# Performance work log

Measured on AMD Instinct MI355X. Metric: run time of the kernel, lower is better.

Reference implementation:

```python
import jax, jax.numpy as jnp
import numpy as np

IN_CH = 512
MID = max(IN_CH // 8, 1)


def setup_inputs() -> dict:
    key = jax.random.key(0)
    ks = jax.random.split(key, 8)
    B, C, H, W = 4, IN_CH, 64, 64
    s = 0.05
    x = jax.random.normal(ks[0], (B, C, H, W), dtype=jnp.float32)
    wq = jax.random.normal(ks[1], (MID, C), dtype=jnp.float32) * s
    bq = jnp.zeros((MID,), dtype=jnp.float32)
    wk = jax.random.normal(ks[2], (MID, C), dtype=jnp.float32) * s
    bk = jnp.zeros((MID,), dtype=jnp.float32)
    wv = jax.random.normal(ks[3], (C, C), dtype=jnp.float32) * s
    bv = jnp.zeros((C,), dtype=jnp.float32)
    alpha = jnp.ones((1,), dtype=jnp.float32) * 0.5  # nonzero so attention path is exercised
    return {"x": x, "wq": wq, "bq": bq, "wk": wk, "bk": bk, "wv": wv, "bv": bv, "alpha": alpha}


def reference(x, wq, bq, wk, bk, wv, bv, alpha):
    B, C, H, W = x.shape
    N = H * W
    xf = x.reshape(B, C, N)  # [B, C, N]
    # 1x1 convs == per-position channel GEMMs
    q = jnp.einsum('mc,bcn->bnm', wq, xf) + bq  # [B, N, mid]
    k = jnp.einsum('mc,bcn->bmn', wk, xf) + bk[None, :, None]  # [B, mid, N]
    v = jnp.einsum('dc,bcn->bdn', wv, xf) + bv[None, :, None]  # [B, C, N]
    attn = jax.nn.softmax(jnp.einsum('bnm,bmk->bnk', q, k), axis=-1)  # [B, N, N]
    out = jnp.einsum('bdn,bkn->bdk', v, attn)  # v @ attn^T -> [B, C, N]
    out = out.reshape(B, C, H, W)
    return alpha * out + x
```

## Files before the change

### kernel.cpp

```cpp
#include <hip/hip_runtime.h>

#define BB 4
#define CD 512
#define NP 4096
#define MID 64
#define PSTR 88

typedef _Float16 half8 __attribute__((ext_vector_type(8)));
typedef _Float16 half4 __attribute__((ext_vector_type(4)));
typedef float floatx4 __attribute__((ext_vector_type(4)));

#define LOG2E 1.4426950408889634f

__global__ __launch_bounds__(256) void prep_w(
    const float* __restrict__ wq, const float* __restrict__ wk,
    const float* __restrict__ wv, const float* __restrict__ bq,
    const float* __restrict__ bk, const float* __restrict__ bv,
    _Float16* __restrict__ w_h, float* __restrict__ bias) {
  int idx = blockIdx.x * 256 + threadIdx.x;
  for (int i = idx; i < 640 * 512; i += gridDim.x * 256) {
    int r = i >> 9, c = i & 511;
    float v = (r < 64) ? wq[(r << 9) + c] * LOG2E
            : (r < 128) ? wk[((r - 64) << 9) + c]
                        : wv[((r - 128) << 9) + c];
    w_h[i] = (_Float16)v;
  }
  if (idx < 640) {
    float v = (idx < 64) ? bq[idx] * LOG2E
            : (idx < 128) ? bk[idx - 64]
                          : bv[idx - 128];
    bias[idx] = v;
  }
}

__global__ __launch_bounds__(256) void transpose_x(const float* __restrict__ x,
                                                   _Float16* __restrict__ xt) {
  __shared__ float tile[64][65];
  int b = blockIdx.z, c0 = blockIdx.y * 64, n0 = blockIdx.x * 64;
  int t = threadIdx.x;
  const float* xb = x + (size_t)b * CD * NP;
#pragma unroll
  for (int k = 0; k < 16; k++) {
    int cl = k * 4 + (t >> 6);
    int nl = t & 63;
    tile[cl][nl] = xb[(size_t)(c0 + cl) * NP + n0 + nl];
  }
  __syncthreads();
  _Float16* xtb = xt + ((size_t)b * NP + n0) * CD + c0;
#pragma unroll
  for (int k = 0; k < 2; k++) {
    int nl = k * 32 + (t >> 3);
    int cl = (t & 7) * 8;
    half8 pk;
#pragma unroll
    for (int i = 0; i < 8; i++) pk[i] = (_Float16)tile[cl + i][nl];
    *(half8*)(xtb + (size_t)nl * CD + cl) = pk;
  }
}

__global__ __launch_bounds__(256, 2) void proj_qkv(
    const _Float16* __restrict__ w_h, const float* __restrict__ bias,
    const _Float16* __restrict__ xt, _Float16* __restrict__ q_h,
    _Float16* __restrict__ k_h, _Float16* __restrict__ v_h) {
  __shared__ _Float16 xls[64 * 512];
  int t = threadIdx.x, w = t >> 6, lane = t & 63;
  int col = lane & 15, quad = lane >> 4;
  int rbh = blockIdx.x, nb = blockIdx.y, b = blockIdx.z;
  int n0 = nb * 64;
  const _Float16* xtb = xt + ((size_t)b * NP + n0) * CD;

#pragma unroll
  for (int j = 0; j < 16; j++) {
    int u = t + j * 256;
    int row = u >> 6, un = u & 63;
    *(half8*)(xls + row * 512 + ((un ^ (row & 7)) << 3)) =
        *(const half8*)(xtb + (size_t)row * CD + un * 8);
  }
  __syncthreads();

  int rw = rbh * 320 + w * 80;
  floatx4 acc[5][4] = {};
  for (int c = 0; c < CD; c += 32) {
    int cu = c >> 3;
    half8 a[5], bf[4];
#pragma unroll
    for (int i = 0; i < 5; i++)
      a[i] = *(const half8*)(w_h + (size_t)(rw + i * 16 + col) * CD + c + quad * 8);
#pragma unroll
    for (int j = 0; j < 4; j++) {
      int row = j * 16 + col;
      bf[j] = *(const half8*)(xls + row * 512 + (((cu + quad) ^ (row & 7)) << 3));
    }
#pragma unroll
    for (int i = 0; i < 5; i++)
#pragma unroll
      for (int j = 0; j < 4; j++)
        acc[i][j] = __builtin_amdgcn_mfma_f32_16x16x32_f16(a[i], bf[j], acc[i][j], 0, 0, 0);
  }

#pragma unroll
  for (int i = 0; i < 5; i++) {
    int r0 = rw + i * 16;
    float bi[4];
#pragma unroll
    for (int rr = 0; rr < 4; rr++) bi[rr] = bias[r0 + quad * 4 + rr];
    if (r0 < 128) {
      _Float16* dst = (r0 < 64 ? q_h + (size_t)b * NP * MID + r0
                               : k_h + (size_t)b * NP * MID + (r0 - 64));
#pragma unroll
      for (int j = 0; j < 4; j++) {
        int n = n0 + j * 16 + col;
        half4 pk;
#pragma unroll
        for (int rr = 0; rr < 4; rr++) pk[rr] = (_Float16)(acc[i][j][rr] + bi[rr]);
        *(half4*)(dst + (size_t)n * MID + quad * 4) = pk;
      }
    } else {
      int dbase = r0 - 128 + quad * 4;
#pragma unroll
      for (int j = 0; j < 4; j++) {
        int n = n0 + j * 16 + col;
#pragma unroll
        for (int rr = 0; rr < 4; rr++)
          v_h[((size_t)b * CD + dbase + rr) * NP + n] =
              (_Float16)(acc[i][j][rr] + bi[rr]);
      }
    }
  }
}

__global__ __launch_bounds__(256) void rowmax(const _Float16* __restrict__ q_h,
                                              const _Float16* __restrict__ k_h,
                                              float* __restrict__ M) {
  int qb = blockIdx.x, b = blockIdx.y;
  int t = threadIdx.x, w = t >> 6, lane = t & 63;
  int col = lane & 15, quad = lane >> 4;
  int q0 = qb * 32;
  const _Float16* qp = q_h + ((size_t)b * NP + q0) * MID;
  half8 bq[2][2];
#pragma unroll
  for (int qt = 0; qt < 2; qt++)
#pragma unroll
    for (int h = 0; h < 2; h++)
      bq[qt][h] = *(const half8*)(qp + (size_t)(qt * 16 + col) * MID + h * 32 + quad * 8);
  const _Float16* kp = k_h + ((size_t)b * NP + (size_t)w * 1024) * MID;
  float m[2] = {-1e30f, -1e30f};
#pragma unroll 4
  for (int n = 0; n < 1024; n += 16) {
    half8 ak0 = *(const half8*)(kp + (size_t)(n + col) * MID + quad * 8);
    half8 ak1 = *(const half8*)(kp + (size_t)(n + col) * MID + 32 + quad * 8);
#pragma unroll
    for (int qt = 0; qt < 2; qt++) {
      floatx4 s = {};
      s = __builtin_amdgcn_mfma_f32_16x16x32_f16(ak0, bq[qt][0], s, 0, 0, 0);
      s = __builtin_amdgcn_mfma_f32_16x16x32_f16(ak1, bq[qt][1], s, 0, 0, 0);
      m[qt] = fmaxf(m[qt], fmaxf(fmaxf(s[0], s[1]), fmaxf(s[2], s[3])));
    }
  }
  __shared__ float red[4][2][16];
#pragma unroll
  for (int qt = 0; qt < 2; qt++) {
    m[qt] = fmaxf(m[qt], __shfl_xor(m[qt], 16));
    m[qt] = fmaxf(m[qt], __shfl_xor(m[qt], 32));
  }
  if (quad == 0) {
    red[w][0][col] = m[0];
    red[w][1][col] = m[1];
  }
  __syncthreads();
  if (t < 32) {
    int qt = t >> 4, c = t & 15;
    float mm = fmaxf(fmaxf(red[0][qt][c], red[1][qt][c]),
                     fmaxf(red[2][qt][c], red[3][qt][c]));
    M[(size_t)b * NP + q0 + t] = mm;
  }
}

__global__ __launch_bounds__(256, 2) void attn_pv(
    const _Float16* __restrict__ q_h, const _Float16* __restrict__ k_h,
    const _Float16* __restrict__ v_h, const float* __restrict__ M,
    const float* __restrict__ x, const float* __restrict__ alpha_p,
    float* __restrict__ out) {
  int bid = blockIdx.x;
  int combo = bid & 7;
  int b = combo >> 1, ds = combo & 1;
  int qb = bid >> 3;
  int q0 = qb * 64, d0 = ds * 256;

  int t = threadIdx.x, w = t >> 6, lane = t & 63;
  int col = lane & 15, quad = lane >> 4;

  __shared__ _Float16 pbuf[2][64 * PSTR];
  __shared__ float lred[4][4][16];
  __shared__ float lfin[64];

  const _Float16* qp = q_h + ((size_t)b * NP + q0) * MID;
  half8 bq[4][2];
#pragma unroll
  for (int qt = 0; qt < 4; qt++)
#pragma unroll
    for (int h = 0; h < 2; h++)
      bq[qt][h] = *(const half8*)(qp + (size_t)(qt * 16 + col) * MID + h * 32 + quad * 8);
  float Mq[4];
#pragma unroll
  for (int qt = 0; qt < 4; qt++) Mq[qt] = M[(size_t)b * NP + q0 + qt * 16 + col];

  const _Float16* kw = k_h + ((size_t)b * NP + w * 16 + col) * MID + quad * 8;
  const _Float16* vp = v_h + ((size_t)(b * CD + d0) + w * 64) * NP;

  floatx4 acc[4][4] = {};
  float lp[4] = {0.f, 0.f, 0.f, 0.f};

  half8 ak0 = *(const half8*)(kw);
  half8 ak1 = *(const half8*)(kw + 32);
  half8 av[2][4];
#pragma unroll
  for (int f = 0; f < 2; f++)
#pragma unroll
    for (int dt = 0; dt < 4; dt++)
      av[f][dt] = *(const half8*)(vp + (size_t)(dt * 16 + col) * NP + f * 32 + quad * 8);

#pragma unroll 2
  for (int ci = 0; ci < 64; ci++) {
    _Float16* pb = pbuf[ci & 1];
    int ncn = ((ci + 1) & 63) * 64;

    half8 an0 = *(const half8*)(kw + (size_t)ncn * MID);
    half8 an1 = *(const half8*)(kw + (size_t)ncn * MID + 32);
    half8 avn[2][4];
#pragma unroll
    for (int f = 0; f < 2; f++)
#pragma unroll
      for (int dt = 0; dt < 4; dt++)
        avn[f][dt] = *(const half8*)(vp + (size_t)(dt * 16 + col) * NP + ncn + f * 32 + quad * 8);

#pragma unroll
    for (int qt = 0; qt < 4; qt++) {
      floatx4 s = {};
      s = __builtin_amdgcn_mfma_f32_16x16x32_f16(ak0, bq[qt][0], s, 0, 0, 0);
      s = __builtin_amdgcn_mfma_f32_16x16x32_f16(ak1, bq[qt][1], s, 0, 0, 0);
      half4 pk;
#pragma unroll
      for (int r = 0; r < 4; r++) {
        float p = __builtin_amdgcn_exp2f(s[r] - Mq[qt]);
        lp[qt] += p;
        pk[r] = (_Float16)p;
      }
      *(half4*)(pb + (qt * 16 + col) * PSTR + w * 16 + quad * 4) = pk;
    }

    asm volatile("s_waitcnt lgkmcnt(0)" ::: "memory");
    __builtin_amdgcn_s_barrier();

    half8 bp[2][4];
#pragma unroll
    for (int f = 0; f < 2; f++)
#pragma unroll
      for (int qt = 0; qt < 4; qt++)
        bp[f][qt] = *(const half8*)(pb + (qt * 16 + col) * PSTR + f * 32 + quad * 8);
    __builtin_amdgcn_s_setprio(1);
#pragma unroll
    for (int f = 0; f < 2; f++)
#pragma unroll
      for (int dt = 0; dt < 4; dt++)
#pragma unroll
        for (int qt = 0; qt < 4; qt++)
          acc[dt][qt] = __builtin_amdgcn_mfma_f32_16x16x32_f16(av[f][dt], bp[f][qt], acc[dt][qt], 0, 0, 0);
    __builtin_amdgcn_s_setprio(0);

    ak0 = an0; ak1 = an1;
#pragma unroll
    for (int f = 0; f < 2; f++)
#pragma unroll
      for (int dt = 0; dt < 4; dt++)
        av[f][dt] = avn[f][dt];
  }

#pragma unroll
  for (int qt = 0; qt < 4; qt++) {
    lp[qt] += __shfl_xor(lp[qt], 16);
    lp[qt] += __shfl_xor(lp[qt], 32);
    if (quad == 0) lred[w][qt][col] = lp[qt];
  }
  __syncthreads();
  if (t < 64) {
    int qt = t >> 4, c = t & 15;
    float l = lred[0][qt][c] + lred[1][qt][c] + lred[2][qt][c] + lred[3][qt][c];
    lfin[t] = alpha_p[0] / l;
  }
  __syncthreads();

  const float* xp = x + ((size_t)(b * CD + d0) + w * 64) * NP;
  float* op = out + ((size_t)(b * CD + d0) + w * 64) * NP;
#pragma unroll
  for (int dt = 0; dt < 4; dt++)
#pragma unroll
    for (int qt = 0; qt < 4; qt++) {
      float linv = lfin[qt * 16 + col];
#pragma unroll
      for (int r = 0; r < 4; r++) {
        size_t o = (size_t)(dt * 16 + quad * 4 + r) * NP + q0 + qt * 16 + col;
        op[o] = acc[dt][qt][r] * linv + xp[o];
      }
    }
}

extern "C" void kernel_launch(void* const* d_in, const int* in_sizes, int n_in,
                              void* d_out, int out_size, void* d_ws, size_t ws_size,
                              hipStream_t stream) {
  const float* x     = (const float*)d_in[0];
  const float* wq    = (const float*)d_in[1];
  const float* bq    = (const float*)d_in[2];
  const float* wk    = (const float*)d_in[3];
  const float* bk    = (const float*)d_in[4];
  const float* wv    = (const float*)d_in[5];
  const float* bv    = (const float*)d_in[6];
  const float* alpha = (const float*)d_in[7];
  float* out = (float*)d_out;

  char* ws = (char*)d_ws;
  _Float16* w_h  = (_Float16*)(ws);
  float*    bias = (float*)(ws + 655360);
  float*    Mbuf = (float*)(ws + 657920);
  _Float16* xt   = (_Float16*)(ws + 723456);
  _Float16* q_h  = (_Float16*)(ws + 17500672);
  _Float16* k_h  = (_Float16*)(ws + 19597824);
  _Float16* v_h  = (_Float16*)(ws + 21694976);

  prep_w<<<1280, 256, 0, stream>>>(wq, wk, wv, bq, bk, bv, w_h, bias);
  transpose_x<<<dim3(64, 8, BB), 256, 0, stream>>>(x, xt);
  proj_qkv<<<dim3(2, 64, BB), 256, 0, stream>>>(w_h, bias, xt, q_h, k_h, v_h);
  rowmax<<<dim3(128, BB), 256, 0, stream>>>(q_h, k_h, Mbuf);
  attn_pv<<<512, 256, 0, stream>>>(q_h, k_h, v_h, Mbuf, x, alpha, out);
}
```

Baseline: 309.0 us.

## Software-pipeline QK^T softmax with PV MMA and swizzle P buffer layout

Restructures the attention loop so that each iteration computes the scores and exponentials for the next key chunk while running the PV MFMAs on the previous chunk's P tile. This leaves one barrier per iteration and lets the exp/softmax work overlap with the matrix math. The padded P shared buffer (stride 88) becomes an unpadded 64-wide layout with an XOR swizzle, which cuts LDS use and aims to avoid bank conflicts. The K prefetch is now two chunks ahead, which raises register pressure at 2 waves/SIMD, and the prologue/epilogue logic is more complex.

After: 312.2 us. About the same (+1.0%).

```diff
diff --git a/kernel.cpp b/kernel.cpp
--- a/kernel.cpp
+++ b/kernel.cpp
@@ -4,7 +4,6 @@
 #define CD 512
 #define NP 4096
 #define MID 64
-#define PSTR 88
 
 typedef _Float16 half8 __attribute__((ext_vector_type(8)));
 typedef _Float16 half4 __attribute__((ext_vector_type(4)));
@@ -189,8 +188,9 @@
 
   int t = threadIdx.x, w = t >> 6, lane = t & 63;
   int col = lane & 15, quad = lane >> 4;
-
-  __shared__ _Float16 pbuf[2][64 * PSTR];
+  int c7 = col & 7;
+
+  __shared__ _Float16 pbuf[2][64 * 64];
   __shared__ float lred[4][4][16];
   __shared__ float lfin[64];
 
@@ -208,37 +208,69 @@
   const _Float16* kw = k_h + ((size_t)b * NP + w * 16 + col) * MID + quad * 8;
   const _Float16* vp = v_h + ((size_t)(b * CD + d0) + w * 64) * NP;
 
+  int wru = (((w * 2 + (quad >> 1)) ^ c7) << 3) + ((quad & 1) << 2);
+  int rdu0 = (((0 * 4 + quad) ^ c7) << 3);
+  int rdu1 = (((1 * 4 + quad) ^ c7) << 3);
+
   floatx4 acc[4][4] = {};
   float lp[4] = {0.f, 0.f, 0.f, 0.f};
 
-  half8 ak0 = *(const half8*)(kw);
-  half8 ak1 = *(const half8*)(kw + 32);
-  half8 av[2][4];
+  half8 akC0 = *(const half8*)(kw);
+  half8 akC1 = *(const half8*)(kw + 32);
+  half8 akN0 = *(const half8*)(kw + (size_t)64 * MID);
+  half8 akN1 = *(const half8*)(kw + (size_t)64 * MID + 32);
+  half8 avC[2][4];
 #pragma unroll
   for (int f = 0; f < 2; f++)
 #pragma unroll
     for (int dt = 0; dt < 4; dt++)
-      av[f][dt] = *(const half8*)(vp + (size_t)(dt * 16 + col) * NP + f * 32 + quad * 8);
-
-#pragma unroll 2
-  for (int ci = 0; ci < 64; ci++) {
-    _Float16* pb = pbuf[ci & 1];
+      avC[f][dt] = *(const half8*)(vp + (size_t)(dt * 16 + col) * NP + f * 32 + quad * 8);
+
+#pragma unroll
+  for (int qt = 0; qt < 4; qt++) {
+    floatx4 s = {};
+    s = __builtin_amdgcn_mfma_f32_16x16x32_f16(akC0, bq[qt][0], s, 0, 0, 0);
+    s = __builtin_amdgcn_mfma_f32_16x16x32_f16(akC1, bq[qt][1], s, 0, 0, 0);
+    half4 pk;
+#pragma unroll
+    for (int r = 0; r < 4; r++) {
+      float p = __builtin_amdgcn_exp2f(s[r] - Mq[qt]);
+      lp[qt] += p;
+      pk[r] = (_Float16)p;
+    }
+    *(half4*)(pbuf[0] + (qt * 16 + col) * 64 + wru) = pk;
+  }
+  asm volatile("s_waitcnt lgkmcnt(0)" ::: "memory");
+  __builtin_amdgcn_s_barrier();
+
+  for (int ci = 1; ci < 64; ci++) {
+    _Float16* pbR = pbuf[(ci - 1) & 1];
+    _Float16* pbW = pbuf[ci & 1];
+    int nc = ci * 64;
+
+    half8 bp[2][4];
+#pragma unroll
+    for (int qt = 0; qt < 4; qt++) {
+      bp[0][qt] = *(const half8*)(pbR + (qt * 16 + col) * 64 + rdu0);
+      bp[1][qt] = *(const half8*)(pbR + (qt * 16 + col) * 64 + rdu1);
+    }
+
     int ncn = ((ci + 1) & 63) * 64;
-
-    half8 an0 = *(const half8*)(kw + (size_t)ncn * MID);
-    half8 an1 = *(const half8*)(kw + (size_t)ncn * MID + 32);
-    half8 avn[2][4];
+    half8 akT0 = akN0, akT1 = akN1;
+    akN0 = *(const half8*)(kw + (size_t)ncn * MID);
+    akN1 = *(const half8*)(kw + (size_t)ncn * MID + 32);
+    half8 avN[2][4];
 #pragma unroll
     for (int f = 0; f < 2; f++)
 #pragma unroll
       for (int dt = 0; dt < 4; dt++)
-        avn[f][dt] = *(const half8*)(vp + (size_t)(dt * 16 + col) * NP + ncn + f * 32 + quad * 8);
+        avN[f][dt] = *(const half8*)(vp + (size_t)(dt * 16 + col) * NP + nc + f * 32 + quad * 8);
 
 #pragma unroll
     for (int qt = 0; qt < 4; qt++) {
       floatx4 s = {};
-      s = __builtin_amdgcn_mfma_f32_16x16x32_f16(ak0, bq[qt][0], s, 0, 0, 0);
-      s = __builtin_amdgcn_mfma_f32_16x16x32_f16(ak1, bq[qt][1], s, 0, 0, 0);
+      s = __builtin_amdgcn_mfma_f32_16x16x32_f16(akT0, bq[qt][0], s, 0, 0, 0);
+      s = __builtin_amdgcn_mfma_f32_16x16x32_f16(akT1, bq[qt][1], s, 0, 0, 0);
       half4 pk;
 #pragma unroll
       for (int r = 0; r < 4; r++) {
@@ -246,34 +278,44 @@
         lp[qt] += p;
         pk[r] = (_Float16)p;
       }
-      *(half4*)(pb + (qt * 16 + col) * PSTR + w * 16 + quad * 4) = pk;
-    }
+      *(half4*)(pbW + (qt * 16 + col) * 64 + wru) = pk;
+    }
+
+    __builtin_amdgcn_s_setprio(1);
+#pragma unroll
+    for (int f = 0; f < 2; f++)
+#pragma unroll
+      for (int dt = 0; dt < 4; dt++)
+#pragma unroll
+        for (int qt = 0; qt < 4; qt++)
+          acc[dt][qt] = __builtin_amdgcn_mfma_f32_16x16x32_f16(avC[f][dt], bp[f][qt], acc[dt][qt], 0, 0, 0);
+    __builtin_amdgcn_s_setprio(0);
 
     asm volatile("s_waitcnt lgkmcnt(0)" ::: "memory");
     __builtin_amdgcn_s_barrier();
 
+#pragma unroll
+    for (int f = 0; f < 2; f++)
+#pragma unroll
+      for (int dt = 0; dt < 4; dt++)
+        avC[f][dt] = avN[f][dt];
+  }
+
+  {
+    _Float16* pbR = pbuf[1];
     half8 bp[2][4];
 #pragma unroll
+    for (int qt = 0; qt < 4; qt++) {
+      bp[0][qt] = *(const half8*)(pbR + (qt * 16 + col) * 64 + rdu0);
+      bp[1][qt] = *(const half8*)(pbR + (qt * 16 + col) * 64 + rdu1);
+    }
+#pragma unroll
     for (int f = 0; f < 2; f++)
 #pragma unroll
-      for (int qt = 0; qt < 4; qt++)
-        bp[f][qt] = *(const half8*)(pb + (qt * 16 + col) * PSTR + f * 32 + quad * 8);
-    __builtin_amdgcn_s_setprio(1);
-#pragma unroll
-    for (int f = 0; f < 2; f++)
-#pragma unroll
       for (int dt = 0; dt < 4; dt++)
 #pragma unroll
         for (int qt = 0; qt < 4; qt++)
-          acc[dt][qt] = __builtin_amdgcn_mfma_f32_16x16x32_f16(av[f][dt], bp[f][qt], acc[dt][qt], 0, 0, 0);
-    __builtin_amdgcn_s_setprio(0);
-
-    ak0 = an0; ak1 = an1;
-#pragma unroll
-    for (int f = 0; f < 2; f++)
-#pragma unroll
-      for (int dt = 0; dt < 4; dt++)
-        av[f][dt] = avn[f][dt];
+          acc[dt][qt] = __builtin_amdgcn_mfma_f32_16x16x32_f16(avC[f][dt], bp[f][qt], acc[dt][qt], 0, 0, 0);
   }
 
 #pragma unroll
```
